# Kernel tuning notes

Measured on AMD Instinct MI355X. Metric: run time of the kernel, lower is better.

## Reference

```python
import jax, jax.numpy as jnp
import numpy as np

T, B = 384, 128
IN_DIM, HID, OUT_DIM = 512, 1024, 512


def _lstm_step(h, c, x_t, Wx, Wh, b):
    # x_t: [B, D], h/c: [B, H]; gates order: i, f, g, o
    gates = x_t @ Wx + h @ Wh + b  # [B, 4H]
    i, f, g, o = jnp.split(gates, 4, axis=-1)
    c_new = jax.nn.sigmoid(f) * c + jax.nn.sigmoid(i) * jnp.tanh(g)
    h_new = jax.nn.sigmoid(o) * jnp.tanh(c_new)
    return h_new, c_new


def setup_inputs() -> dict:
    key = jax.random.key(0)
    ks = jax.random.split(key, 9)
    s_in = 1.0 / np.sqrt(IN_DIM)
    s_h = 1.0 / np.sqrt(HID)
    s_o = 1.0 / np.sqrt(OUT_DIM)
    return {
        "x": jax.random.normal(ks[0], (T, B, IN_DIM), dtype=jnp.float32),
        "hidden_state": jnp.zeros((1, B, HID), dtype=jnp.float32),
        "cell_state": jnp.zeros((1, B, HID), dtype=jnp.float32),
        "enc_Wx": jax.random.normal(ks[1], (IN_DIM, 4 * HID), dtype=jnp.float32) * s_in,
        "enc_Wh": jax.random.normal(ks[2], (HID, 4 * HID), dtype=jnp.float32) * s_h,
        "enc_b": jnp.zeros((4 * HID,), dtype=jnp.float32),
        "dec_Wx": jax.random.normal(ks[3], (OUT_DIM, 4 * HID), dtype=jnp.float32) * s_o,
        "dec_Wh": jax.random.normal(ks[4], (HID, 4 * HID), dtype=jnp.float32) * s_h,
        "dec_b": jnp.zeros((4 * HID,), dtype=jnp.float32),
        "fc_W": jax.random.normal(ks[5], (HID, OUT_DIM), dtype=jnp.float32) * s_h,
        "fc_b": jnp.zeros((OUT_DIM,), dtype=jnp.float32),
    }


def reference(x, hidden_state, cell_state, enc_Wx, enc_Wh, enc_b,
              dec_Wx, dec_Wh, dec_b, fc_W, fc_b):
    # ---- encoder: run LSTM over T steps, keep only final hidden state ----
    h0, c0 = hidden_state[0], cell_state[0]  # [B, H]

    def enc_step(carry, x_t):
        h, c = carry
        h, c = _lstm_step(h, c, x_t, enc_Wx, enc_Wh, enc_b)
        return (h, c), None

    (h_enc, _), _ = jax.lax.scan(enc_step, (h0, c0), x)

    y0 = jnp.zeros((B, OUT_DIM), dtype=x.dtype)
    c_dec0 = jnp.zeros((B, HID), dtype=x.dtype)

    def dec_step(carry, _):
        y, h, c = carry
        h, c = _lstm_step(h, c, y, dec_Wx, dec_Wh, dec_b)
        y = jax.nn.softmax(h @ fc_W + fc_b, axis=-1)  # softmax over dim=2
        return (y, h, c), y

    _, output = jax.lax.scan(dec_step, (y0, h_enc, c_dec0), None, length=T)
    return output  # [T, B, OUT_DIM]
```

## Files before the change

kernel.cpp:

```cpp
#include <hip/hip_runtime.h>


#define TS 384

typedef __attribute__((ext_vector_type(8))) short bf16x8;
typedef __attribute__((ext_vector_type(4))) float f32x4;

#define WS_XR 4096u
#define XR_SLOT 262144u
#define WS_HP (WS_XR + 4u*XR_SLOT)
#define HP_BUF 524288u
#define WS_FPN (WS_HP + 2u*HP_BUF)
#define WS_TOTAL (WS_FPN + 2097152u)

#define MFMA __builtin_amdgcn_mfma_f32_16x16x32_bf16

__device__ __forceinline__ unsigned short bf16r(float v) {
  unsigned u = __float_as_uint(v);
  u += 0x7FFFu + ((u >> 16) & 1u);
  return (unsigned short)(u >> 16);
}
__device__ __forceinline__ float bf2f(unsigned short h) {
  return __uint_as_float(((unsigned)h) << 16);
}
__device__ __forceinline__ void split2(float v, short& hi, short& lo) {
  unsigned short h = bf16r(v);
  float r = v - bf2f(h);
  hi = (short)h; lo = (short)bf16r(r);
}
__device__ __forceinline__ float sigm(float v)  { return 1.0f / (1.0f + __expf(-v)); }
__device__ __forceinline__ float tanhfa(float v){ return 1.0f - 2.0f / (__expf(2.0f*v) + 1.0f); }

__device__ __forceinline__ void st_u64(void* p, unsigned long long v) {
  __hip_atomic_store((unsigned long long*)p, v, __ATOMIC_RELAXED, __HIP_MEMORY_SCOPE_AGENT);
}
__device__ __forceinline__ unsigned long long ld_u64(const void* p) {
  return __hip_atomic_load((const unsigned long long*)p, __ATOMIC_RELAXED, __HIP_MEMORY_SCOPE_AGENT);
}
__device__ __forceinline__ void st_u32(unsigned* p, unsigned v) {
  __hip_atomic_store(p, v, __ATOMIC_RELAXED, __HIP_MEMORY_SCOPE_AGENT);
}
__device__ __forceinline__ unsigned ld_u32(const unsigned* p) {
  return __hip_atomic_load(p, __ATOMIC_RELAXED, __HIP_MEMORY_SCOPE_AGENT);
}
__device__ __forceinline__ void st_f32(float* p, float v) {
  __hip_atomic_store(p, v, __ATOMIC_RELAXED, __HIP_MEMORY_SCOPE_AGENT);
}
__device__ __forceinline__ float ld_f32(const float* p) {
  return __hip_atomic_load(p, __ATOMIC_RELAXED, __HIP_MEMORY_SCOPE_AGENT);
}

__device__ __forceinline__ void setflag(unsigned* flag, unsigned val) {
  asm volatile("s_waitcnt vmcnt(0)" ::: "memory");
  __syncthreads();
  if (threadIdx.x == 0)
    __hip_atomic_store(flag, val, __ATOMIC_RELAXED, __HIP_MEMORY_SCOPE_AGENT);
}
__device__ __forceinline__ void hwait(const unsigned* flags, unsigned* invdone_line,
                                      bool leader, unsigned target, int* sDead) {
  if (leader) {
    if (threadIdx.x < 64) {
      const unsigned long long* q = (const unsigned long long*)(flags + threadIdx.x * 4);
      unsigned spins = 0;
      for (;;) {
        unsigned long long q0 = ld_u64(q), q1 = ld_u64(q + 1);
        bool ok = ((unsigned)q0 >= target) && ((unsigned)(q0 >> 32) >= target)
               && ((unsigned)q1 >= target) && ((unsigned)(q1 >> 32) >= target);
        if (__all(ok)) break;
        if (++spins > (1u << 20)) { if (threadIdx.x == 0) *sDead = 1; break; }
      }
    }
    if (threadIdx.x == 0) {
      __builtin_amdgcn_fence(__ATOMIC_ACQUIRE, "agent");
      st_u32(invdone_line, target);
      asm volatile("s_waitcnt vmcnt(0)" ::: "memory");
    }
  } else {
    if (threadIdx.x == 0) {
      unsigned spins = 0;
      while (ld_u32(invdone_line) < target) {
        if (++spins > (1u << 20)) { *sDead = 1; break; }
      }
      asm volatile("buffer_inv sc0" ::: "memory");
      asm volatile("s_waitcnt vmcnt(0)" ::: "memory");
    }
  }
  __syncthreads();
}
__device__ __forceinline__ void wait128(const unsigned* flags, unsigned target, int* sDead) {
  if (threadIdx.x < 64) {
    const int i = threadIdx.x;
    const bool act = (i * 4) < 128;
    const unsigned long long* q = (const unsigned long long*)(flags + i * 4);
    unsigned spins = 0;
    for (;;) {
      bool ok = true;
      if (act) {
        unsigned long long q0 = ld_u64(q), q1 = ld_u64(q + 1);
        ok = ((unsigned)q0 >= target) && ((unsigned)(q0 >> 32) >= target)
          && ((unsigned)q1 >= target) && ((unsigned)(q1 >> 32) >= target);
      }
      if (__all(ok)) break;
      if (++spins > (1u << 20)) { if (i == 0) *sDead = 1; break; }
    }
  }
  __syncthreads();
}

__device__ void load_gate_weights(const float* __restrict__ Wx, const float* __restrict__ Wh,
                                  int p, short* sBh, short* sBl) {
  for (int idx = threadIdx.x; idx < 24576; idx += 1024) {
    int j = idx & 7, l = (idx >> 3) & 63, kb = idx >> 9;
    int k = kb * 32 + ((l >> 4) << 3) + j;
    int c = l & 15;
    int gcol = (c >> 2) * 1024 + p * 4 + (c & 3);
    float wv = (k < 512) ? Wx[(size_t)k * 4096 + gcol]
                         : Wh[(size_t)(k - 512) * 4096 + gcol];
    short hi, lo; split2(wv, hi, lo);
    sBh[idx] = hi; sBl[idx] = lo;
  }
}
__device__ void load_fc_weights(const float* __restrict__ fcW, int kg, int cg,
                                short* sFh, short* sFl) {
  for (int idx = threadIdx.x; idx < 4096; idx += 1024) {
    int j = idx & 7, l = (idx >> 3) & 63, kb = idx >> 9;
    int unit = kg * 256 + kb * 32 + ((l >> 4) << 3) + j;
    int col = cg * 16 + (l & 15);
    short hi, lo; split2(fcW[(size_t)unit * 512 + col], hi, lo);
    sFh[idx] = hi; sFl[idx] = lo;
  }
}

template<int NKB, int D>
__device__ __forceinline__ void gg_pipe(const short* AH_, const short* AL_,
    const short* BH_, const short* BL_, int mt, int l,
    int kbA0, int kbB0, f32x4* acc)
{
  const bf16x8* AH = (const bf16x8*)AH_;
  const bf16x8* AL = (const bf16x8*)AL_;
  const bf16x8* BH = (const bf16x8*)BH_;
  const bf16x8* BL = (const bf16x8*)BL_;
  bf16x8 pah[D], pal[D];
  #pragma unroll
  for (int i = 0; i < D; ++i) {
    pah[i] = AH[((kbA0 + i) * 8 + mt) * 64 + l];
    pal[i] = AL[((kbA0 + i) * 8 + mt) * 64 + l];
  }
  #pragma unroll
  for (int i = 0; i < NKB; ++i) {
    bf16x8 ah = pah[i % D], al = pal[i % D];
    if (i + D < NKB) {
      pah[i % D] = AH[((kbA0 + i + D) * 8 + mt) * 64 + l];
      pal[i % D] = AL[((kbA0 + i + D) * 8 + mt) * 64 + l];
    }
    bf16x8 bh = BH[(kbB0 + i) * 64 + l];
    bf16x8 bl = BL[(kbB0 + i) * 64 + l];
    const int a = (i & 1) * 3;
    acc[a + 0] = MFMA(ah, bh, acc[a + 0], 0, 0, 0);
    acc[a + 1] = MFMA(ah, bl, acc[a + 1], 0, 0, 0);
    acc[a + 2] = MFMA(al, bh, acc[a + 2], 0, 0, 0);
  }
}
__device__ __forceinline__ void gg_finish(f32x4* acc, int kh, int mt, int l,
                                          float* LDSgate) {
  f32x4 s = (acc[0] + acc[3]) + ((acc[1] + acc[4]) + (acc[2] + acc[5]));
  const int col = l & 15, r0 = mt * 16 + ((l >> 4) << 2);
  float* plane = LDSgate + kh * 2176;
  #pragma unroll
  for (int j = 0; j < 4; ++j) plane[(r0 + j) * 17 + col] = s[j];
}

__device__ __forceinline__ void conv_x(const float* __restrict__ xsrc,
                                       short* dstH, short* dstL, int p, int tl) {
  if (tl < 32) {
    int g = p * 32 + tl;
    int l = g & 63, mt = (g >> 6) & 7, kb = g >> 9;
    int row = mt * 16 + (l & 15), k = kb * 32 + ((l >> 4) << 3);
    const float* xs = xsrc + (size_t)row * 512 + k;
    unsigned long long h64[2] = {0, 0}, l64[2] = {0, 0};
    #pragma unroll
    for (int j = 0; j < 8; ++j) {
      short hi, lo; split2(xs[j], hi, lo);
      h64[j >> 2] |= (unsigned long long)(unsigned short)hi << ((j & 3) * 16);
      l64[j >> 2] |= (unsigned long long)(unsigned short)lo << ((j & 3) * 16);
    }
    int off = g * 8;
    st_u64(dstH + off, h64[0]); st_u64(dstH + off + 4, h64[1]);
    st_u64(dstL + off, l64[0]); st_u64(dstL + off + 4, l64[1]);
  }
}

__global__ void __launch_bounds__(1024, 1)
lstm12(const float* __restrict__ x, const float* __restrict__ h0p,
       const float* __restrict__ c0p, const float* __restrict__ eWx,
       const float* __restrict__ eWh, const float* __restrict__ eb,
       const float* __restrict__ dWx, const float* __restrict__ dWh,
       const float* __restrict__ db, const float* __restrict__ fcW,
       const float* __restrict__ fcb, float* __restrict__ out,
       char* __restrict__ ws)
{
  __shared__ __align__(16) short sBh[24576], sBl[24576];
  __shared__ __align__(16) short sFh[4096], sFl[4096];
  __shared__ float LDSgate[2 * 2176];
  __shared__ unsigned hsplit[512];
  __shared__ float ybuf[512];
  __shared__ float red[16];
  __shared__ int sDead, sLeader, sXcd;

  const int p = blockIdx.x, t = threadIdx.x;
  const int w = t >> 6, l = t & 63;
  const int mt = w & 7, kh = w >> 3;
  if (t == 0) sDead = 0;

  unsigned* hflag = (unsigned*)ws;
  unsigned* yflag = (unsigned*)(ws + 1024);
  unsigned* fflag = (unsigned*)(ws + 2048);
  unsigned* elect = (unsigned*)(ws + 3264);

  if (t == 0) {
    unsigned xcd;
    asm volatile("s_getreg_b32 %0, hwreg(HW_REG_XCC_ID)" : "=s"(xcd));
    xcd &= 7u;
    sXcd = (int)xcd;
    unsigned old = __hip_atomic_fetch_add(&elect[xcd], 1u, __ATOMIC_ACQ_REL,
                                          __HIP_MEMORY_SCOPE_AGENT);
    sLeader = (old == 0u) ? 1 : 0;
  }
  __syncthreads();
  const bool leader = (sLeader != 0);
  unsigned* invd = (unsigned*)(ws + 3328 + sXcd * 64);

  short* xrH[4]; short* xrL[4];
  #pragma unroll
  for (int s4 = 0; s4 < 4; ++s4) {
    xrH[s4] = (short*)(ws + WS_XR + s4 * XR_SLOT);
    xrL[s4] = (short*)(ws + WS_XR + s4 * XR_SLOT + 131072u);
  }
  short* hpH[2]; short* hpL[2];
  #pragma unroll
  for (int b2 = 0; b2 < 2; ++b2) {
    hpH[b2] = (short*)(ws + WS_HP + b2 * HP_BUF);
    hpL[b2] = (short*)(ws + WS_HP + b2 * HP_BUF + 262144u);
  }
  float* fp = (float*)(ws + WS_FPN);

  const int row_pw = t & 127, u_pw = (t >> 7) & 3;

  load_gate_weights(eWx, eWh, p, sBh, sBl);
  conv_x(x, xrH[0], xrL[0], p, t);
  conv_x(x + 65536, xrH[1], xrL[1], p, t);
  if (t < 64) {
    int hg = p * 64 + t;
    int ll = hg & 63, mtt = (hg >> 6) & 7, hk = hg >> 9;
    int row = mtt * 16 + (ll & 15), k = hk * 32 + ((ll >> 4) << 3);
    const float* hs = h0p + (size_t)row * 1024 + k;
    unsigned long long h64[2] = {0, 0}, l64[2] = {0, 0};
    #pragma unroll
    for (int j = 0; j < 8; ++j) {
      short hi, lo; split2(hs[j], hi, lo);
      h64[j >> 2] |= (unsigned long long)(unsigned short)hi << ((j & 3) * 16);
      l64[j >> 2] |= (unsigned long long)(unsigned short)lo << ((j & 3) * 16);
    }
    int off = hg * 8;
    st_u64(hpH[0] + off, h64[0]); st_u64(hpH[0] + off + 4, h64[1]);
    st_u64(hpL[0] + off, l64[0]); st_u64(hpL[0] + off + 4, l64[1]);
  }
  float creg = 0.f, bq0 = 0.f, bq1 = 0.f, bq2 = 0.f, bq3 = 0.f;
  if (t < 512) {
    creg = c0p[(size_t)row_pw * 1024 + p * 4 + u_pw];
    bq0 = eb[0 * 1024 + p * 4 + u_pw];
    bq1 = eb[1 * 1024 + p * 4 + u_pw];
    bq2 = eb[2 * 1024 + p * 4 + u_pw];
    bq3 = eb[3 * 1024 + p * 4 + u_pw];
  }
  setflag(&hflag[p], 1u);
  hwait(hflag, invd, leader, 1u, &sDead);
  if (sDead) return;

  for (int st = 0; st < TS; ++st) {
    int rb = st & 1, wb = rb ^ 1, xs = st & 3;
    f32x4 z = {0.f, 0.f, 0.f, 0.f};
    f32x4 acc[6] = {z, z, z, z, z, z};
    gg_pipe<8, 4>(xrH[xs], xrL[xs], sBh, sBl, mt, l, kh * 8, kh * 8, acc);
    hwait(hflag, invd, leader, (unsigned)(st + 1), &sDead);
    if (sDead) return;
    gg_pipe<16, 4>(hpH[rb], hpL[rb], sBh, sBl, mt, l, kh * 16, 16 + kh * 16, acc);
    gg_finish(acc, kh, mt, l, LDSgate);
    __syncthreads();
    if (t < 512) {
      float g0 = LDSgate[row_pw * 17 + 0  + u_pw] + LDSgate[2176 + row_pw * 17 + 0  + u_pw] + bq0;
      float g1 = LDSgate[row_pw * 17 + 4  + u_pw] + LDSgate[2176 + row_pw * 17 + 4  + u_pw] + bq1;
      float g2 = LDSgate[row_pw * 17 + 8  + u_pw] + LDSgate[2176 + row_pw * 17 + 8  + u_pw] + bq2;
      float g3 = LDSgate[row_pw * 17 + 12 + u_pw] + LDSgate[2176 + row_pw * 17 + 12 + u_pw] + bq3;
      creg = sigm(g1) * creg + sigm(g0) * tanhfa(g2);
      float h = sigm(g3) * tanhfa(creg);
      short hi, lo; split2(h, hi, lo);
      hsplit[u_pw * 128 + row_pw] = ((unsigned)(unsigned short)hi << 16) | (unsigned short)lo;
    } else if (st + 2 < TS) {
      conv_x(x + (size_t)(st + 2) * 65536, xrH[(st + 2) & 3], xrL[(st + 2) & 3], p, t - 512);
    }
    __syncthreads();
    if (t < 128) {
      int r = t;
      unsigned w0 = hsplit[r], w1 = hsplit[128 + r], w2 = hsplit[256 + r], w3 = hsplit[384 + r];
      unsigned long long hi64 = (unsigned long long)(w0 >> 16)
        | ((unsigned long long)(w1 >> 16) << 16)
        | ((unsigned long long)(w2 >> 16) << 32)
        | ((unsigned long long)(w3 >> 16) << 48);
      unsigned long long lo64 = (unsigned long long)(w0 & 0xFFFFu)
        | ((unsigned long long)(w1 & 0xFFFFu) << 16)
        | ((unsigned long long)(w2 & 0xFFFFu) << 32)
        | ((unsigned long long)(w3 & 0xFFFFu) << 48);
      int hk = p >> 3, mtt = r >> 4;
      int lane_ = (((p >> 1) & 3) << 4) | (r & 15);
      int off = ((hk * 8 + mtt) * 64 + lane_) * 8 + (p & 1) * 4;
      st_u64(hpH[wb] + off, hi64);
      st_u64(hpL[wb] + off, lo64);
    }
    setflag(&hflag[p], (unsigned)(st + 2));
  }

  load_gate_weights(dWx, dWh, p, sBh, sBl);
  if (p >= 128) load_fc_weights(fcW, (p - 128) >> 5, (p - 128) & 31, sFh, sFl);
  if (t < 32) {
    int off = (p * 32 + t) * 8;
    st_u64(xrH[0] + off, 0ull); st_u64(xrH[0] + off + 4, 0ull);
    st_u64(xrL[0] + off, 0ull); st_u64(xrL[0] + off + 4, 0ull);
  }
  creg = 0.0f;
  if (t < 512) {
    bq0 = db[0 * 1024 + p * 4 + u_pw];
    bq1 = db[1 * 1024 + p * 4 + u_pw];
    bq2 = db[2 * 1024 + p * 4 + u_pw];
    bq3 = db[3 * 1024 + p * 4 + u_pw];
  }
  float fcb_r = (t < 512) ? fcb[t] : 0.f;
  setflag(&hflag[p], (unsigned)(TS + 2));

  const unsigned DB = (unsigned)(TS + 2);
  for (int st = 0; st < TS; ++st) {
    const int rb = st & 1, wb = rb ^ 1;
    f32x4 z = {0.f, 0.f, 0.f, 0.f};
    f32x4 acc[6] = {z, z, z, z, z, z};
    hwait(hflag, invd, leader, DB + (unsigned)st, &sDead);
    if (sDead) return;
    if (p >= 128) {
      const int f = p - 128, kg = f >> 5, cg = f & 31;
      if (st >= 1) {
        const bf16x8* AH = (const bf16x8*)hpH[rb];
        const bf16x8* AL = (const bf16x8*)hpL[rb];
        const bf16x8* FB = (const bf16x8*)sFh;
        const bf16x8* FL = (const bf16x8*)sFl;
        f32x4 a0 = z, a1 = z, a2 = z;
        #pragma unroll
        for (int kb = 0; kb < 4; ++kb) {
          int gkb = kg * 8 + kh * 4 + kb;
          bf16x8 ah = AH[(gkb * 8 + mt) * 64 + l];
          bf16x8 al = AL[(gkb * 8 + mt) * 64 + l];
          bf16x8 bh = FB[(kh * 4 + kb) * 64 + l];
          bf16x8 bl = FL[(kh * 4 + kb) * 64 + l];
          a0 = MFMA(ah, bh, a0, 0, 0, 0);
          a1 = MFMA(ah, bl, a1, 0, 0, 0);
          a2 = MFMA(al, bh, a2, 0, 0, 0);
        }
        f32x4 s = a0 + (a1 + a2);
        int slice = kg * 2 + kh;
        int col = cg * 16 + (l & 15), r0 = mt * 16 + ((l >> 4) << 2);
        #pragma unroll
        for (int j = 0; j < 4; ++j)
          st_f32(&fp[(size_t)(slice * 128 + r0 + j) * 512 + col], s[j]);
        setflag(&fflag[f], (unsigned)st);
      }
      gg_pipe<16, 4>(hpH[rb], hpL[rb], sBh, sBl, mt, l, kh * 16, 16 + kh * 16, acc);
      if (st >= 1) { wait128(yflag, (unsigned)st, &sDead); if (sDead) return; }
      gg_pipe<8, 4>(xrH[rb], xrL[rb], sBh, sBl, mt, l, kh * 8, kh * 8, acc);
    } else {
      gg_pipe<16, 4>(hpH[rb], hpL[rb], sBh, sBl, mt, l, kh * 16, 16 + kh * 16, acc);
      if (st >= 1) {
        wait128(fflag, (unsigned)st, &sDead);
        if (sDead) return;
        float v = 0.f, e = 0.f, mx;
        if (t < 512) {
          float tv[8];
          #pragma unroll
          for (int s8 = 0; s8 < 8; ++s8)
            tv[s8] = ld_f32(&fp[(size_t)(s8 * 128 + p) * 512 + t]);
          v = fcb_r + ((tv[0] + tv[1]) + (tv[2] + tv[3]))
                    + ((tv[4] + tv[5]) + (tv[6] + tv[7]));
          mx = v;
          #pragma unroll
          for (int o = 32; o > 0; o >>= 1) mx = fmaxf(mx, __shfl_xor(mx, o));
          if (l == 0) red[w] = mx;
        }
        __syncthreads();
        if (t < 512) {
          mx = red[0];
          #pragma unroll
          for (int i = 1; i < 8; ++i) mx = fmaxf(mx, red[i]);
          e = __expf(v - mx);
          float ss = e;
          #pragma unroll
          for (int o = 32; o > 0; o >>= 1) ss += __shfl_xor(ss, o);
          if (l == 0) red[8 + w] = ss;
        }
        __syncthreads();
        if (t < 512) {
          float ss = (red[8] + red[9]) + (red[10] + red[11])
                   + (red[12] + red[13]) + (red[14] + red[15]);
          float y = e / ss;
          st_f32(&out[((size_t)(st - 1) * 128 + p) * 512 + t], y);
          ybuf[t] = y;
        }
        __syncthreads();
        if (t < 64) {
          int kb = t >> 2, seg = t & 3;
          int k = kb * 32 + seg * 8;
          int lane_ = (seg << 4) | (p & 15), mtt = p >> 4;
          int off = ((kb * 8 + mtt) * 64 + lane_) * 8;
          unsigned long long h64[2] = {0, 0}, l64[2] = {0, 0};
          #pragma unroll
          for (int j = 0; j < 8; ++j) {
            short hi, lo; split2(ybuf[k + j], hi, lo);
            h64[j >> 2] |= (unsigned long long)(unsigned short)hi << ((j & 3) * 16);
            l64[j >> 2] |= (unsigned long long)(unsigned short)lo << ((j & 3) * 16);
          }
          st_u64(xrH[rb] + off, h64[0]); st_u64(xrH[rb] + off + 4, h64[1]);
          st_u64(xrL[rb] + off, l64[0]); st_u64(xrL[rb] + off + 4, l64[1]);
        }
        setflag(&yflag[p], (unsigned)st);
        wait128(yflag, (unsigned)st, &sDead);
        if (sDead) return;
      }
      gg_pipe<8, 4>(xrH[rb], xrL[rb], sBh, sBl, mt, l, kh * 8, kh * 8, acc);
    }
    gg_finish(acc, kh, mt, l, LDSgate);
    __syncthreads();
    if (t < 512) {
      float g0 = LDSgate[row_pw * 17 + 0  + u_pw] + LDSgate[2176 + row_pw * 17 + 0  + u_pw] + bq0;
      float g1 = LDSgate[row_pw * 17 + 4  + u_pw] + LDSgate[2176 + row_pw * 17 + 4  + u_pw] + bq1;
      float g2 = LDSgate[row_pw * 17 + 8  + u_pw] + LDSgate[2176 + row_pw * 17 + 8  + u_pw] + bq2;
      float g3 = LDSgate[row_pw * 17 + 12 + u_pw] + LDSgate[2176 + row_pw * 17 + 12 + u_pw] + bq3;
      creg = sigm(g1) * creg + sigm(g0) * tanhfa(g2);
      float h = sigm(g3) * tanhfa(creg);
      short hi, lo; split2(h, hi, lo);
      hsplit[u_pw * 128 + row_pw] = ((unsigned)(unsigned short)hi << 16) | (unsigned short)lo;
    }
    __syncthreads();
    if (t < 128) {
      int r = t;
      unsigned w0 = hsplit[r], w1 = hsplit[128 + r], w2 = hsplit[256 + r], w3 = hsplit[384 + r];
      unsigned long long hi64 = (unsigned long long)(w0 >> 16)
        | ((unsigned long long)(w1 >> 16) << 16)
        | ((unsigned long long)(w2 >> 16) << 32)
        | ((unsigned long long)(w3 >> 16) << 48);
      unsigned long long lo64 = (unsigned long long)(w0 & 0xFFFFu)
        | ((unsigned long long)(w1 & 0xFFFFu) << 16)
        | ((unsigned long long)(w2 & 0xFFFFu) << 32)
        | ((unsigned long long)(w3 & 0xFFFFu) << 48);
      int hk = p >> 3, mtt = r >> 4;
      int lane_ = (((p >> 1) & 3) << 4) | (r & 15);
      int off = ((hk * 8 + mtt) * 64 + lane_) * 8 + (p & 1) * 4;
      st_u64(hpH[wb] + off, hi64);
      st_u64(hpL[wb] + off, lo64);
    }
    setflag(&hflag[p], DB + (unsigned)(st + 1));
  }

  {
    const int rb = TS & 1;
    hwait(hflag, invd, leader, DB + (unsigned)TS, &sDead);
    if (sDead) return;
    if (p >= 128) {
      const int f = p - 128, kg = f >> 5, cg = f & 31;
      const bf16x8* AH = (const bf16x8*)hpH[rb];
      const bf16x8* AL = (const bf16x8*)hpL[rb];
      const bf16x8* FB = (const bf16x8*)sFh;
      const bf16x8* FL = (const bf16x8*)sFl;
      f32x4 z = {0.f, 0.f, 0.f, 0.f};
      f32x4 a0 = z, a1 = z, a2 = z;
      #pragma unroll
      for (int kb = 0; kb < 4; ++kb) {
        int gkb = kg * 8 + kh * 4 + kb;
        bf16x8 ah = AH[(gkb * 8 + mt) * 64 + l];
        bf16x8 al = AL[(gkb * 8 + mt) * 64 + l];
        bf16x8 bh = FB[(kh * 4 + kb) * 64 + l];
        bf16x8 bl = FL[(kh * 4 + kb) * 64 + l];
        a0 = MFMA(ah, bh, a0, 0, 0, 0);
        a1 = MFMA(ah, bl, a1, 0, 0, 0);
        a2 = MFMA(al, bh, a2, 0, 0, 0);
      }
      f32x4 s = a0 + (a1 + a2);
      int slice = kg * 2 + kh;
      int col = cg * 16 + (l & 15), r0 = mt * 16 + ((l >> 4) << 2);
      #pragma unroll
      for (int j = 0; j < 4; ++j)
        st_f32(&fp[(size_t)(slice * 128 + r0 + j) * 512 + col], s[j]);
      setflag(&fflag[f], (unsigned)TS);
    } else {
      wait128(fflag, (unsigned)TS, &sDead);
      if (sDead) return;
      float v = 0.f, e = 0.f, mx;
      if (t < 512) {
        float tv[8];
        #pragma unroll
        for (int s8 = 0; s8 < 8; ++s8)
          tv[s8] = ld_f32(&fp[(size_t)(s8 * 128 + p) * 512 + t]);
        v = fcb_r + ((tv[0] + tv[1]) + (tv[2] + tv[3]))
                  + ((tv[4] + tv[5]) + (tv[6] + tv[7]));
        mx = v;
        #pragma unroll
        for (int o = 32; o > 0; o >>= 1) mx = fmaxf(mx, __shfl_xor(mx, o));
        if (l == 0) red[w] = mx;
      }
      __syncthreads();
      if (t < 512) {
        mx = red[0];
        #pragma unroll
        for (int i = 1; i < 8; ++i) mx = fmaxf(mx, red[i]);
        e = __expf(v - mx);
        float ss = e;
        #pragma unroll
        for (int o = 32; o > 0; o >>= 1) ss += __shfl_xor(ss, o);
        if (l == 0) red[8 + w] = ss;
      }
      __syncthreads();
      if (t < 512) {
        float ss = (red[8] + red[9]) + (red[10] + red[11])
                 + (red[12] + red[13]) + (red[14] + red[15]);
        st_f32(&out[((size_t)(TS - 1) * 128 + p) * 512 + t], e / ss);
      }
    }
  }
}

extern "C" void kernel_launch(void* const* d_in, const int* in_sizes, int n_in,
                              void* d_out, int out_size, void* d_ws, size_t ws_size,
                              hipStream_t stream) {
  const float* x   = (const float*)d_in[0];
  const float* h0  = (const float*)d_in[1];
  const float* c0  = (const float*)d_in[2];
  const float* eWx = (const float*)d_in[3];
  const float* eWh = (const float*)d_in[4];
  const float* eb  = (const float*)d_in[5];
  const float* dWx = (const float*)d_in[6];
  const float* dWh = (const float*)d_in[7];
  const float* db  = (const float*)d_in[8];
  const float* fcW = (const float*)d_in[9];
  const float* fcb = (const float*)d_in[10];
  float* out = (float*)d_out;

  if (ws_size < (size_t)WS_TOTAL) {
    hipMemsetAsync(d_out, 0xFF, (size_t)out_size * sizeof(float), stream);
    return;
  }
  hipMemsetAsync(d_ws, 0, 4096, stream);
  hipLaunchKernelGGL(lstm12, dim3(256), dim3(1024), 0, stream,
                     x, h0, c0, eWx, eWh, eb, dWx, dWh, db, fcW, fcb, out,
                     (char*)d_ws);
}
```

Before: 13.74 ms.

## Split persistent LSTM across 512 blocks of 512 threads with narrower per-block slices

Repartitions the persistent cooperative LSTM kernel from 256 blocks of 1024 threads to 512 blocks of 512 threads, each owning 2 hidden units instead of 4. The K-split across two wave groups is removed so each wave covers the full K range, and the LDS weight layout is reorganised to match. FC work moves to 256 blocks, each computing two full output columns, so the softmax blocks no longer sum 8 partial slices. More blocks spread the per-step matvec across more CUs, but grid-wide flag polling now spans 512 flags, and the serial K loop per wave is longer.

```diff
diff --git a/kernel.cpp b/kernel.cpp
--- a/kernel.cpp
+++ b/kernel.cpp
@@ -6,14 +6,15 @@
 typedef __attribute__((ext_vector_type(8))) short bf16x8;
 typedef __attribute__((ext_vector_type(4))) float f32x4;
 
-#define WS_XR 4096u
+#define WS_XR 8192u
 #define XR_SLOT 262144u
 #define WS_HP (WS_XR + 4u*XR_SLOT)
 #define HP_BUF 524288u
 #define WS_FPN (WS_HP + 2u*HP_BUF)
-#define WS_TOTAL (WS_FPN + 2097152u)
+#define WS_TOTAL (WS_FPN + 262144u)
 
 #define MFMA __builtin_amdgcn_mfma_f32_16x16x32_bf16
+#define SPINCAP (1u << 22)
 
 __device__ __forceinline__ unsigned short bf16r(float v) {
   unsigned u = __float_as_uint(v);
@@ -56,30 +57,34 @@
   if (threadIdx.x == 0)
     __hip_atomic_store(flag, val, __ATOMIC_RELAXED, __HIP_MEMORY_SCOPE_AGENT);
 }
-__device__ __forceinline__ void hwait(const unsigned* flags, unsigned* invdone_line,
+__device__ __forceinline__ void hwait(const unsigned* flags, unsigned* invd,
                                       bool leader, unsigned target, int* sDead) {
+  const int t = threadIdx.x;
   if (leader) {
-    if (threadIdx.x < 64) {
-      const unsigned long long* q = (const unsigned long long*)(flags + threadIdx.x * 4);
+    if (t < 64) {
+      const unsigned long long* q = (const unsigned long long*)(flags + t * 8);
       unsigned spins = 0;
       for (;;) {
-        unsigned long long q0 = ld_u64(q), q1 = ld_u64(q + 1);
+        unsigned long long q0 = ld_u64(q),     q1 = ld_u64(q + 1);
+        unsigned long long q2 = ld_u64(q + 2), q3 = ld_u64(q + 3);
         bool ok = ((unsigned)q0 >= target) && ((unsigned)(q0 >> 32) >= target)
-               && ((unsigned)q1 >= target) && ((unsigned)(q1 >> 32) >= target);
+               && ((unsigned)q1 >= target) && ((unsigned)(q1 >> 32) >= target)
+               && ((unsigned)q2 >= target) && ((unsigned)(q2 >> 32) >= target)
+               && ((unsigned)q3 >= target) && ((unsigned)(q3 >> 32) >= target);
         if (__all(ok)) break;
-        if (++spins > (1u << 20)) { if (threadIdx.x == 0) *sDead = 1; break; }
-      }
-    }
-    if (threadIdx.x == 0) {
+        if (++spins > SPINCAP) { if (t == 0) *sDead = 1; break; }
+      }
+    }
+    if (t == 0) {
       __builtin_amdgcn_fence(__ATOMIC_ACQUIRE, "agent");
-      st_u32(invdone_line, target);
+      st_u32(invd, target);
       asm volatile("s_waitcnt vmcnt(0)" ::: "memory");
     }
   } else {
-    if (threadIdx.x == 0) {
+    if (t == 0) {
       unsigned spins = 0;
-      while (ld_u32(invdone_line) < target) {
-        if (++spins > (1u << 20)) { *sDead = 1; break; }
+      while (ld_u32(invd) < target) {
+        if (++spins > SPINCAP) { *sDead = 1; break; }
       }
       asm volatile("buffer_inv sc0" ::: "memory");
       asm volatile("s_waitcnt vmcnt(0)" ::: "memory");
@@ -87,59 +92,59 @@
   }
   __syncthreads();
 }
-__device__ __forceinline__ void wait128(const unsigned* flags, unsigned target, int* sDead) {
-  if (threadIdx.x < 64) {
-    const int i = threadIdx.x;
-    const bool act = (i * 4) < 128;
-    const unsigned long long* q = (const unsigned long long*)(flags + i * 4);
+template<int NF>
+__device__ __forceinline__ void waitN(const unsigned* flags, unsigned target, int* sDead) {
+  const int t = threadIdx.x;
+  if (t < 64) {
+    constexpr int PU = NF / 128;
+    const unsigned long long* q = (const unsigned long long*)(flags + t * (PU * 2));
     unsigned spins = 0;
     for (;;) {
       bool ok = true;
-      if (act) {
-        unsigned long long q0 = ld_u64(q), q1 = ld_u64(q + 1);
-        ok = ((unsigned)q0 >= target) && ((unsigned)(q0 >> 32) >= target)
-          && ((unsigned)q1 >= target) && ((unsigned)(q1 >> 32) >= target);
+      #pragma unroll
+      for (int i = 0; i < PU; ++i) {
+        unsigned long long v = ld_u64(q + i);
+        if (!(((unsigned)v >= target) && ((unsigned)(v >> 32) >= target))) ok = false;
       }
       if (__all(ok)) break;
-      if (++spins > (1u << 20)) { if (i == 0) *sDead = 1; break; }
+      if (++spins > SPINCAP) { if (t == 0) *sDead = 1; break; }
     }
   }
   __syncthreads();
 }
 
-__device__ void load_gate_weights(const float* __restrict__ Wx, const float* __restrict__ Wh,
-                                  int p, short* sBh, short* sBl) {
-  for (int idx = threadIdx.x; idx < 24576; idx += 1024) {
-    int j = idx & 7, l = (idx >> 3) & 63, kb = idx >> 9;
-    int k = kb * 32 + ((l >> 4) << 3) + j;
-    int c = l & 15;
-    int gcol = (c >> 2) * 1024 + p * 4 + (c & 3);
+__device__ void load_gw(const float* __restrict__ Wx, const float* __restrict__ Wh,
+                        int p, short* sBh, short* sBl) {
+  for (int idx = threadIdx.x; idx < 12288; idx += 512) {
+    int kb = idx >> 8, rem = idx & 255;
+    int c8 = rem >> 5, kk = rem & 31;
+    int k = kb * 32 + kk;
+    int gcol = (c8 >> 1) * 1024 + p * 2 + (c8 & 1);
     float wv = (k < 512) ? Wx[(size_t)k * 4096 + gcol]
                          : Wh[(size_t)(k - 512) * 4096 + gcol];
     short hi, lo; split2(wv, hi, lo);
     sBh[idx] = hi; sBl[idx] = lo;
   }
 }
-__device__ void load_fc_weights(const float* __restrict__ fcW, int kg, int cg,
-                                short* sFh, short* sFl) {
-  for (int idx = threadIdx.x; idx < 4096; idx += 1024) {
-    int j = idx & 7, l = (idx >> 3) & 63, kb = idx >> 9;
-    int unit = kg * 256 + kb * 32 + ((l >> 4) << 3) + j;
-    int col = cg * 16 + (l & 15);
+__device__ void load_fcw(const float* __restrict__ fcW, int f, short* sFh, short* sFl) {
+  for (int idx = threadIdx.x; idx < 2048; idx += 512) {
+    int kb = idx >> 6, rem = idx & 63;
+    int c = rem >> 5, kk = rem & 31;
+    int unit = kb * 32 + kk;
+    int col = f * 2 + c;
     short hi, lo; split2(fcW[(size_t)unit * 512 + col], hi, lo);
     sFh[idx] = hi; sFl[idx] = lo;
   }
 }
 
 template<int NKB, int D>
-__device__ __forceinline__ void gg_pipe(const short* AH_, const short* AL_,
+__device__ __forceinline__ void gg(const short* AH_, const short* AL_,
     const short* BH_, const short* BL_, int mt, int l,
     int kbA0, int kbB0, f32x4* acc)
 {
   const bf16x8* AH = (const bf16x8*)AH_;
   const bf16x8* AL = (const bf16x8*)AL_;
-  const bf16x8* BH = (const bf16x8*)BH_;
-  const bf16x8* BL = (const bf16x8*)BL_;
+  const int boff = ((l & 7) * 32) + ((l >> 4) << 3);
   bf16x8 pah[D], pal[D];
   #pragma unroll
   for (int i = 0; i < D; ++i) {
@@ -153,27 +158,28 @@
       pah[i % D] = AH[((kbA0 + i + D) * 8 + mt) * 64 + l];
       pal[i % D] = AL[((kbA0 + i + D) * 8 + mt) * 64 + l];
     }
-    bf16x8 bh = BH[(kbB0 + i) * 64 + l];
-    bf16x8 bl = BL[(kbB0 + i) * 64 + l];
+    bf16x8 bh = *(const bf16x8*)&BH_[(kbB0 + i) * 256 + boff];
+    bf16x8 bl = *(const bf16x8*)&BL_[(kbB0 + i) * 256 + boff];
     const int a = (i & 1) * 3;
     acc[a + 0] = MFMA(ah, bh, acc[a + 0], 0, 0, 0);
     acc[a + 1] = MFMA(ah, bl, acc[a + 1], 0, 0, 0);
     acc[a + 2] = MFMA(al, bh, acc[a + 2], 0, 0, 0);
   }
 }
-__device__ __forceinline__ void gg_finish(f32x4* acc, int kh, int mt, int l,
-                                          float* LDSgate) {
+__device__ __forceinline__ void gg_finish(f32x4* acc, int mt, int l, float* LDSgate) {
   f32x4 s = (acc[0] + acc[3]) + ((acc[1] + acc[4]) + (acc[2] + acc[5]));
-  const int col = l & 15, r0 = mt * 16 + ((l >> 4) << 2);
-  float* plane = LDSgate + kh * 2176;
-  #pragma unroll
-  for (int j = 0; j < 4; ++j) plane[(r0 + j) * 17 + col] = s[j];
+  const int col8 = l & 15;
+  if (col8 < 8) {
+    const int r0 = mt * 16 + ((l >> 4) << 2);
+    #pragma unroll
+    for (int j = 0; j < 4; ++j) LDSgate[(r0 + j) * 9 + col8] = s[j];
+  }
 }
 
 __device__ __forceinline__ void conv_x(const float* __restrict__ xsrc,
                                        short* dstH, short* dstL, int p, int tl) {
-  if (tl < 32) {
-    int g = p * 32 + tl;
+  if (tl >= 0 && tl < 16) {
+    int g = p * 16 + tl;
     int l = g & 63, mt = (g >> 6) & 7, kb = g >> 9;
     int row = mt * 16 + (l & 15), k = kb * 32 + ((l >> 4) << 3);
     const float* xs = xsrc + (size_t)row * 512 + k;
@@ -190,8 +196,8 @@
   }
 }
 
-__global__ void __launch_bounds__(1024, 1)
-lstm12(const float* __restrict__ x, const float* __restrict__ h0p,
+__global__ void __launch_bounds__(512, 4)
+lstm17(const float* __restrict__ x, const float* __restrict__ h0p,
        const float* __restrict__ c0p, const float* __restrict__ eWx,
        const float* __restrict__ eWh, const float* __restrict__ eb,
        const float* __restrict__ dWx, const float* __restrict__ dWh,
@@ -199,23 +205,23 @@
        const float* __restrict__ fcb, float* __restrict__ out,
        char* __restrict__ ws)
 {
-  __shared__ __align__(16) short sBh[24576], sBl[24576];
-  __shared__ __align__(16) short sFh[4096], sFl[4096];
-  __shared__ float LDSgate[2 * 2176];
-  __shared__ unsigned hsplit[512];
+  __shared__ __align__(16) short sBh[12288], sBl[12288];
+  __shared__ __align__(16) short sFh[2048], sFl[2048];
+  __shared__ float LDSgate[128 * 9];
+  __shared__ unsigned hsplit[256];
   __shared__ float ybuf[512];
   __shared__ float red[16];
   __shared__ int sDead, sLeader, sXcd;
 
   const int p = blockIdx.x, t = threadIdx.x;
   const int w = t >> 6, l = t & 63;
-  const int mt = w & 7, kh = w >> 3;
+  const int mt = w;
   if (t == 0) sDead = 0;
 
   unsigned* hflag = (unsigned*)ws;
-  unsigned* yflag = (unsigned*)(ws + 1024);
-  unsigned* fflag = (unsigned*)(ws + 2048);
-  unsigned* elect = (unsigned*)(ws + 3264);
+  unsigned* yflag = (unsigned*)(ws + 2048);
+  unsigned* fflag = (unsigned*)(ws + 2560);
+  unsigned* elect = (unsigned*)(ws + 3584);
 
   if (t == 0) {
     unsigned xcd;
@@ -228,7 +234,7 @@
   }
   __syncthreads();
   const bool leader = (sLeader != 0);
-  unsigned* invd = (unsigned*)(ws + 3328 + sXcd * 64);
+  unsigned* invd = (unsigned*)(ws + 3648 + sXcd * 64);
 
   short* xrH[4]; short* xrL[4];
   #pragma unroll
@@ -244,13 +250,13 @@
   }
   float* fp = (float*)(ws + WS_FPN);
 
-  const int row_pw = t & 127, u_pw = (t >> 7) & 3;
-
-  load_gate_weights(eWx, eWh, p, sBh, sBl);
+  const int row_pw = t & 127, u_pw = (t >> 7) & 1;
+
+  load_gw(eWx, eWh, p, sBh, sBl);
   conv_x(x, xrH[0], xrL[0], p, t);
-  conv_x(x + 65536, xrH[1], xrL[1], p, t);
-  if (t < 64) {
-    int hg = p * 64 + t;
+  conv_x(x + 65536, xrH[1], xrL[1], p, (t >= 16 && t < 32) ? (t - 16) : -1);
+  if (t < 32) {
+    int hg = p * 32 + t;
     int ll = hg & 63, mtt = (hg >> 6) & 7, hk = hg >> 9;
     int row = mtt * 16 + (ll & 15), k = hk * 32 + ((ll >> 4) << 3);
     const float* hs = h0p + (size_t)row * 1024 + k;
@@ -266,12 +272,11 @@
     st_u64(hpL[0] + off, l64[0]); st_u64(hpL[0] + off + 4, l64[1]);
   }
   float creg = 0.f, bq0 = 0.f, bq1 = 0.f, bq2 = 0.f, bq3 = 0.f;
-  if (t < 512) {
-    creg = c0p[(size_t)row_pw * 1024 + p * 4 + u_pw];
-    bq0 = eb[0 * 1024 + p * 4 + u_pw];
-    bq1 = eb[1 * 1024 + p * 4 + u_pw];
-    bq2 = eb[2 * 1024 + p * 4 + u_pw];
-    bq3 = eb[3 * 1024 + p * 4 + u_pw];
+  if (t < 256) {
+    int ug = p * 2 + u_pw;
+    creg = c0p[(size_t)row_pw * 1024 + ug];
+    bq0 = eb[0 * 1024 + ug]; bq1 = eb[1 * 1024 + ug];
+    bq2 = eb[2 * 1024 + ug]; bq3 = eb[3 * 1024 + ug];
   }
   setflag(&hflag[p], 1u);
   hwait(hflag, invd, leader, 1u, &sDead);
@@ -281,60 +286,54 @@
     int rb = st & 1, wb = rb ^ 1, xs = st & 3;
     f32x4 z = {0.f, 0.f, 0.f, 0.f};
     f32x4 acc[6] = {z, z, z, z, z, z};
-    gg_pipe<8, 4>(xrH[xs], xrL[xs], sBh, sBl, mt, l, kh * 8, kh * 8, acc);
+    gg<16, 4>(xrH[xs], xrL[xs], sBh, sBl, mt, l, 0, 0, acc);
     hwait(hflag, invd, leader, (unsigned)(st + 1), &sDead);
     if (sDead) return;
-    gg_pipe<16, 4>(hpH[rb], hpL[rb], sBh, sBl, mt, l, kh * 16, 16 + kh * 16, acc);
-    gg_finish(acc, kh, mt, l, LDSgate);
+    gg<32, 4>(hpH[rb], hpL[rb], sBh, sBl, mt, l, 0, 16, acc);
+    gg_finish(acc, mt, l, LDSgate);
     __syncthreads();
-    if (t < 512) {
-      float g0 = LDSgate[row_pw * 17 + 0  + u_pw] + LDSgate[2176 + row_pw * 17 + 0  + u_pw] + bq0;
-      float g1 = LDSgate[row_pw * 17 + 4  + u_pw] + LDSgate[2176 + row_pw * 17 + 4  + u_pw] + bq1;
-      float g2 = LDSgate[row_pw * 17 + 8  + u_pw] + LDSgate[2176 + row_pw * 17 + 8  + u_pw] + bq2;
-      float g3 = LDSgate[row_pw * 17 + 12 + u_pw] + LDSgate[2176 + row_pw * 17 + 12 + u_pw] + bq3;
+    if (t < 256) {
+      float g0 = LDSgate[row_pw * 9 + 0 + u_pw] + bq0;
+      float g1 = LDSgate[row_pw * 9 + 2 + u_pw] + bq1;
+      float g2 = LDSgate[row_pw * 9 + 4 + u_pw] + bq2;
+      float g3 = LDSgate[row_pw * 9 + 6 + u_pw] + bq3;
       creg = sigm(g1) * creg + sigm(g0) * tanhfa(g2);
       float h = sigm(g3) * tanhfa(creg);
       short hi, lo; split2(h, hi, lo);
       hsplit[u_pw * 128 + row_pw] = ((unsigned)(unsigned short)hi << 16) | (unsigned short)lo;
     } else if (st + 2 < TS) {
-      conv_x(x + (size_t)(st + 2) * 65536, xrH[(st + 2) & 3], xrL[(st + 2) & 3], p, t - 512);
+      conv_x(x + (size_t)(st + 2) * 65536, xrH[(st + 2) & 3], xrL[(st + 2) & 3], p, t - 256);
     }
     __syncthreads();
     if (t < 128) {
       int r = t;
-      unsigned w0 = hsplit[r], w1 = hsplit[128 + r], w2 = hsplit[256 + r], w3 = hsplit[384 + r];
-      unsigned long long hi64 = (unsigned long long)(w0 >> 16)
-        | ((unsigned long long)(w1 >> 16) << 16)
-        | ((unsigned long long)(w2 >> 16) << 32)
-        | ((unsigned long long)(w3 >> 16) << 48);
-      unsigned long long lo64 = (unsigned long long)(w0 & 0xFFFFu)
-        | ((unsigned long long)(w1 & 0xFFFFu) << 16)
-        | ((unsigned long long)(w2 & 0xFFFFu) << 32)
-        | ((unsigned long long)(w3 & 0xFFFFu) << 48);
-      int hk = p >> 3, mtt = r >> 4;
-      int lane_ = (((p >> 1) & 3) << 4) | (r & 15);
-      int off = ((hk * 8 + mtt) * 64 + lane_) * 8 + (p & 1) * 4;
-      st_u64(hpH[wb] + off, hi64);
-      st_u64(hpL[wb] + off, lo64);
+      unsigned h0v = hsplit[r], h1v = hsplit[128 + r];
+      unsigned hi32 = (h0v >> 16) | ((h1v >> 16) << 16);
+      unsigned lo32 = (h0v & 0xFFFFu) | ((h1v & 0xFFFFu) << 16);
+      int kb = p >> 4, mtt = r >> 4;
+      int lane_ = (((p >> 2) & 3) << 4) | (r & 15);
+      int j = (p * 2) & 7;
+      int off = ((kb * 8 + mtt) * 64 + lane_) * 8 + j;
+      st_u32((unsigned*)(hpH[wb] + off), hi32);
+      st_u32((unsigned*)(hpL[wb] + off), lo32);
     }
     setflag(&hflag[p], (unsigned)(st + 2));
   }
 
-  load_gate_weights(dWx, dWh, p, sBh, sBl);
-  if (p >= 128) load_fc_weights(fcW, (p - 128) >> 5, (p - 128) & 31, sFh, sFl);
-  if (t < 32) {
-    int off = (p * 32 + t) * 8;
+  load_gw(dWx, dWh, p, sBh, sBl);
+  if (p >= 256) load_fcw(fcW, p - 256, sFh, sFl);
+  if (t < 16) {
+    int off = (p * 16 + t) * 8;
     st_u64(xrH[0] + off, 0ull); st_u64(xrH[0] + off + 4, 0ull);
     st_u64(xrL[0] + off, 0ull); st_u64(xrL[0] + off + 4, 0ull);
   }
   creg = 0.0f;
-  if (t < 512) {
-    bq0 = db[0 * 1024 + p * 4 + u_pw];
-    bq1 = db[1 * 1024 + p * 4 + u_pw];
-    bq2 = db[2 * 1024 + p * 4 + u_pw];
-    bq3 = db[3 * 1024 + p * 4 + u_pw];
-  }
-  float fcb_r = (t < 512) ? fcb[t] : 0.f;
+  if (t < 256) {
+    int ug = p * 2 + u_pw;
+    bq0 = db[0 * 1024 + ug]; bq1 = db[1 * 1024 + ug];
+    bq2 = db[2 * 1024 + ug]; bq3 = db[3 * 1024 + ug];
+  }
+  float fcb_r = fcb[t];
   setflag(&hflag[p], (unsigned)(TS + 2));
 
   const unsigned DB = (unsigned)(TS + 2);
@@ -344,73 +343,66 @@
     f32x4 acc[6] = {z, z, z, z, z, z};
     hwait(hflag, invd, leader, DB + (unsigned)st, &sDead);
     if (sDead) return;
-    if (p >= 128) {
-      const int f = p - 128, kg = f >> 5, cg = f & 31;
+    if (p >= 256) {
       if (st >= 1) {
+        const int boff2 = ((l & 1) * 32) + ((l >> 4) << 3);
         const bf16x8* AH = (const bf16x8*)hpH[rb];
         const bf16x8* AL = (const bf16x8*)hpL[rb];
-        const bf16x8* FB = (const bf16x8*)sFh;
-        const bf16x8* FL = (const bf16x8*)sFl;
-        f32x4 a0 = z, a1 = z, a2 = z;
+        f32x4 a0 = z, a1 = z, a2 = z, a3 = z, a4 = z, a5 = z;
         #pragma unroll
-        for (int kb = 0; kb < 4; ++kb) {
-          int gkb = kg * 8 + kh * 4 + kb;
-          bf16x8 ah = AH[(gkb * 8 + mt) * 64 + l];
-          bf16x8 al = AL[(gkb * 8 + mt) * 64 + l];
-          bf16x8 bh = FB[(kh * 4 + kb) * 64 + l];
-          bf16x8 bl = FL[(kh * 4 + kb) * 64 + l];
-          a0 = MFMA(ah, bh, a0, 0, 0, 0);
-          a1 = MFMA(ah, bl, a1, 0, 0, 0);
-          a2 = MFMA(al, bh, a2, 0, 0, 0);
+        for (int kb = 0; kb < 32; ++kb) {
+          bf16x8 ah = AH[(kb * 8 + mt) * 64 + l];
+          bf16x8 al = AL[(kb * 8 + mt) * 64 + l];
+          bf16x8 bh = *(const bf16x8*)&sFh[kb * 64 + boff2];
+          bf16x8 bl = *(const bf16x8*)&sFl[kb * 64 + boff2];
+          if ((kb & 1) == 0) {
+            a0 = MFMA(ah, bh, a0, 0, 0, 0);
+            a1 = MFMA(ah, bl, a1, 0, 0, 0);
+            a2 = MFMA(al, bh, a2, 0, 0, 0);
+          } else {
+            a3 = MFMA(ah, bh, a3, 0, 0, 0);
+            a4 = MFMA(ah, bl, a4, 0, 0, 0);
+            a5 = MFMA(al, bh, a5, 0, 0, 0);
+          }
         }
-        f32x4 s = a0 + (a1 + a2);
-        int slice = kg * 2 + kh;
-        int col = cg * 16 + (l & 15), r0 = mt * 16 + ((l >> 4) << 2);
+        f32x4 s = (a0 + a3) + ((a1 + a4) + (a2 + a5));
+        if ((l & 15) < 2) {
+          int col = (p - 256) * 2 + (l & 1);
+          int r0 = mt * 16 + ((l >> 4) << 2);
+          #pragma unroll
+          for (int j = 0; j < 4; ++j)
+            st_f32(&fp[(size_t)(r0 + j) * 512 + col], s[j]);
+        }
+        setflag(&fflag[p - 256], (unsigned)st);
+      }
+      gg<32, 4>(hpH[rb], hpL[rb], sBh, sBl, mt, l, 0, 16, acc);
+      if (st >= 1) { waitN<128>(yflag, (unsigned)st, &sDead); if (sDead) return; }
+      gg<16, 4>(xrH[rb], xrL[rb], sBh, sBl, mt, l, 0, 0, acc);
+    } else {
+      gg<32, 4>(hpH[rb], hpL[rb], sBh, sBl, mt, l, 0, 16, acc);
+      if (p < 128 && st >= 1) {
+        waitN<256>(fflag, (unsigned)st, &sDead);
+        if (sDead) return;
+        float v = fcb_r + ld_f32(&fp[(size_t)p * 512 + t]);
+        float mx = v;
         #pragma unroll
-        for (int j = 0; j < 4; ++j)
-          st_f32(&fp[(size_t)(slice * 128 + r0 + j) * 512 + col], s[j]);
-        setflag(&fflag[f], (unsigned)st);
-      }
-      gg_pipe<16, 4>(hpH[rb], hpL[rb], sBh, sBl, mt, l, kh * 16, 16 + kh * 16, acc);
-      if (st >= 1) { wait128(yflag, (unsigned)st, &sDead); if (sDead) return; }
-      gg_pipe<8, 4>(xrH[rb], xrL[rb], sBh, sBl, mt, l, kh * 8, kh * 8, acc);
-    } else {
-      gg_pipe<16, 4>(hpH[rb], hpL[rb], sBh, sBl, mt, l, kh * 16, 16 + kh * 16, acc);
-      if (st >= 1) {
-        wait128(fflag, (unsigned)st, &sDead);
-        if (sDead) return;
-        float v = 0.f, e = 0.f, mx;
-        if (t < 512) {
-          float tv[8];
-          #pragma unroll
-          for (int s8 = 0; s8 < 8; ++s8)
-            tv[s8] = ld_f32(&fp[(size_t)(s8 * 128 + p) * 512 + t]);
-          v = fcb_r + ((tv[0] + tv[1]) + (tv[2] + tv[3]))
-                    + ((tv[4] + tv[5]) + (tv[6] + tv[7]));
-          mx = v;
-          #pragma unroll
-          for (int o = 32; o > 0; o >>= 1) mx = fmaxf(mx, __shfl_xor(mx, o));
-          if (l == 0) red[w] = mx;
-        }
+        for (int o = 32; o > 0; o >>= 1) mx = fmaxf(mx, __shfl_xor(mx, o));
+        if (l == 0) red[w] = mx;
         __syncthreads();
-        if (t < 512) {
-          mx = red[0];
-          #pragma unroll
-          for (int i = 1; i < 8; ++i) mx = fmaxf(mx, red[i]);
-          e = __expf(v - mx);
-          float ss = e;
-          #pragma unroll
-          for (int o = 32; o > 0; o >>= 1) ss += __shfl_xor(ss, o);
-          if (l == 0) red[8 + w] = ss;
-        }
+        mx = red[0];
+        #pragma unroll
+        for (int i = 1; i < 8; ++i) mx = fmaxf(mx, red[i]);
+        float e = __expf(v - mx);
+        float ss = e;
+        #pragma unroll
+        for (int o = 32; o > 0; o >>= 1) ss += __shfl_xor(ss, o);
+        if (l == 0) red[8 + w] = ss;
         __syncthreads();
-        if (t < 512) {
-          float ss = (red[8] + red[9]) + (red[10] + red[11])
-                   + (red[12] + red[13]) + (red[14] + red[15]);
-          float y = e / ss;
-          st_f32(&out[((size_t)(st - 1) * 128 + p) * 512 + t], y);
-          ybuf[t] = y;
-        }
+        ss = (red[8] + red[9]) + (red[10] + red[11])
+           + (red[12] + red[13]) + (red[14] + red[15]);
+        float y = e / ss;
+        st_f32(&out[((size_t)(st - 1) * 128 + p) * 512 + t], y);
+        ybuf[t] = y;
         __syncthreads();
         if (t < 64) {
           int kb = t >> 2, seg = t & 3;
@@ -428,18 +420,17 @@
           st_u64(xrL[rb] + off, l64[0]); st_u64(xrL[rb] + off + 4, l64[1]);
         }
         setflag(&yflag[p], (unsigned)st);
-        wait128(yflag, (unsigned)st, &sDead);
-        if (sDead) return;
-      }
-      gg_pipe<8, 4>(xrH[rb], xrL[rb], sBh, sBl, mt, l, kh * 8, kh * 8, acc);
-    }
-    gg_finish(acc, kh, mt, l, LDSgate);
+      }
+      if (st >= 1) { waitN<128>(yflag, (unsigned)st, &sDead); if (sDead) return; }
+      gg<16, 4>(xrH[rb], xrL[rb], sBh, sBl, mt, l, 0, 0, acc);
+    }
+    gg_finish(acc, mt, l, LDSgate);
     __syncthreads();
-    if (t < 512) {
-      float g0 = LDSgate[row_pw * 17 + 0  + u_pw] + LDSgate[2176 + row_pw * 17 + 0  + u_pw] + bq0;
-      float g1 = LDSgate[row_pw * 17 + 4  + u_pw] + LDSgate[2176 + row_pw * 17 + 4  + u_pw] + bq1;
-      float g2 = LDSgate[row_pw * 17 + 8  + u_pw] + LDSgate[2176 + row_pw * 17 + 8  + u_pw] + bq2;
-      float g3 = LDSgate[row_pw * 17 + 12 + u_pw] + LDSgate[2176 + row_pw * 17 + 12 + u_pw] + bq3;
+    if (t < 256) {
+      float g0 = LDSgate[row_pw * 9 + 0 + u_pw] + bq0;
+      float g1 = LDSgate[row_pw * 9 + 2 + u_pw] + bq1;
+      float g2 = LDSgate[row_pw * 9 + 4 + u_pw] + bq2;
+      float g3 = LDSgate[row_pw * 9 + 6 + u_pw] + bq3;
       creg = sigm(g1) * creg + sigm(g0) * tanhfa(g2);
       float h = sigm(g3) * tanhfa(creg);
       short hi, lo; split2(h, hi, lo);
@@ -448,20 +439,15 @@
     __syncthreads();
     if (t < 128) {
       int r = t;
-      unsigned w0 = hsplit[r], w1 = hsplit[128 + r], w2 = hsplit[256 + r], w3 = hsplit[384 + r];
-      unsigned long long hi64 = (unsigned long long)(w0 >> 16)
-        | ((unsigned long long)(w1 >> 16) << 16)
-        | ((unsigned long long)(w2 >> 16) << 32)
-        | ((unsigned long long)(w3 >> 16) << 48);
-      unsigned long long lo64 = (unsigned long long)(w0 & 0xFFFFu)
-        | ((unsigned long long)(w1 & 0xFFFFu) << 16)
-        | ((unsigned long long)(w2 & 0xFFFFu) << 32)
-        | ((unsigned long long)(w3 & 0xFFFFu) << 48);
-      int hk = p >> 3, mtt = r >> 4;
-      int lane_ = (((p >> 1) & 3) << 4) | (r & 15);
-      int off = ((hk * 8 + mtt) * 64 + lane_) * 8 + (p & 1) * 4;
-      st_u64(hpH[wb] + off, hi64);
-      st_u64(hpL[wb] + off, lo64);
+      unsigned h0v = hsplit[r], h1v = hsplit[128 + r];
+      unsigned hi32 = (h0v >> 16) | ((h1v >> 16) << 16);
+      unsigned lo32 = (h0v & 0xFFFFu) | ((h1v & 0xFFFFu) << 16);
+      int kb = p >> 4, mtt = r >> 4;
+      int lane_ = (((p >> 2) & 3) << 4) | (r & 15);
+      int j = (p * 2) & 7;
+      int off = ((kb * 8 + mtt) * 64 + lane_) * 8 + j;
+      st_u32((unsigned*)(hpH[wb] + off), hi32);
+      st_u32((unsigned*)(hpL[wb] + off), lo32);
     }
     setflag(&hflag[p], DB + (unsigned)(st + 1));
   }
@@ -470,65 +456,58 @@
     const int rb = TS & 1;
     hwait(hflag, invd, leader, DB + (unsigned)TS, &sDead);
     if (sDead) return;
-    if (p >= 128) {
-      const int f = p - 128, kg = f >> 5, cg = f & 31;
+    if (p >= 256) {
+      const int boff2 = ((l & 1) * 32) + ((l >> 4) << 3);
       const bf16x8* AH = (const bf16x8*)hpH[rb];
       const bf16x8* AL = (const bf16x8*)hpL[rb];
-      const bf16x8* FB = (const bf16x8*)sFh;
-      const bf16x8* FL = (const bf16x8*)sFl;
       f32x4 z = {0.f, 0.f, 0.f, 0.f};
-      f32x4 a0 = z, a1 = z, a2 = z;
+      f32x4 a0 = z, a1 = z, a2 = z, a3 = z, a4 = z, a5 = z;
       #pragma unroll
-      for (int kb = 0; kb < 4; ++kb) {
-        int gkb = kg * 8 + kh * 4 + kb;
-        bf16x8 ah = AH[(gkb * 8 + mt) * 64 + l];
-        bf16x8 al = AL[(gkb * 8 + mt) * 64 + l];
-        bf16x8 bh = FB[(kh * 4 + kb) * 64 + l];
-        bf16x8 bl = FL[(kh * 4 + kb) * 64 + l];
-        a0 = MFMA(ah, bh, a0, 0, 0, 0);
-        a1 = MFMA(ah, bl, a1, 0, 0, 0);
-        a2 = MFMA(al, bh, a2, 0, 0, 0);
-      }
-      f32x4 s = a0 + (a1 + a2);
-      int slice = kg * 2 + kh;
-      int col = cg * 16 + (l & 15), r0 = mt * 16 + ((l >> 4) << 2);
+      for (int kb = 0; kb < 32; ++kb) {
+        bf16x8 ah = AH[(kb * 8 + mt) * 64 + l];
+        bf16x8 al = AL[(kb * 8 + mt) * 64 + l];
+        bf16x8 bh = *(const bf16x8*)&sFh[kb * 64 + boff2];
+        bf16x8 bl = *(const bf16x8*)&sFl[kb * 64 + boff2];
+        if ((kb & 1) == 0) {
+          a0 = MFMA(ah, bh, a0, 0, 0, 0);
+          a1 = MFMA(ah, bl, a1, 0, 0, 0);
+          a2 = MFMA(al, bh, a2, 0, 0, 0);
+        } else {
+          a3 = MFMA(ah, bh, a3, 0, 0, 0);
+          a4 = MFMA(ah, bl, a4, 0, 0, 0);
+          a5 = MFMA(al, bh, a5, 0, 0, 0);
+        }
+      }
+      f32x4 s = (a0 + a3) + ((a1 + a4) + (a2 + a5));
+      if ((l & 15) < 2) {
+        int col = (p - 256) * 2 + (l & 1);
+        int r0 = mt * 16 + ((l >> 4) << 2);
+        #pragma unroll
+        for (int j = 0; j < 4; ++j)
+          st_f32(&fp[(size_t)(r0 + j) * 512 + col], s[j]);
+      }
+      setflag(&fflag[p - 256], (unsigned)TS);
+    } else if (p < 128) {
+      waitN<256>(fflag, (unsigned)TS, &sDead);
+      if (sDead) return;
+      float v = fcb_r + ld_f32(&fp[(size_t)p * 512 + t]);
+      float mx = v;
       #pragma unroll
-      for (int j = 0; j < 4; ++j)
-        st_f32(&fp[(size_t)(slice * 128 + r0 + j) * 512 + col], s[j]);
-      setflag(&fflag[f], (unsigned)TS);
-    } else {
-      wait128(fflag, (unsigned)TS, &sDead);
-      if (sDead) return;
-      float v = 0.f, e = 0.f, mx;
-      if (t < 512) {
-        float tv[8];
-        #pragma unroll
-        for (int s8 = 0; s8 < 8; ++s8)
-          tv[s8] = ld_f32(&fp[(size_t)(s8 * 128 + p) * 512 + t]);
-        v = fcb_r + ((tv[0] + tv[1]) + (tv[2] + tv[3]))
-                  + ((tv[4] + tv[5]) + (tv[6] + tv[7]));
-        mx = v;
-        #pragma unroll
-        for (int o = 32; o > 0; o >>= 1) mx = fmaxf(mx, __shfl_xor(mx, o));
-        if (l == 0) red[w] = mx;
-      }
+      for (int o = 32; o > 0; o >>= 1) mx = fmaxf(mx, __shfl_xor(mx, o));
+      if (l == 0) red[w] = mx;
       __syncthreads();
-      if (t < 512) {
-        mx = red[0];
-        #pragma unroll
-        for (int i = 1; i < 8; ++i) mx = fmaxf(mx, red[i]);
-        e = __expf(v - mx);
-        float ss = e;
-        #pragma unroll
-        for (int o = 32; o > 0; o >>= 1) ss += __shfl_xor(ss, o);
-        if (l == 0) red[8 + w] = ss;
-      }
+      mx = red[0];
+      #pragma unroll
+      for (int i = 1; i < 8; ++i) mx = fmaxf(mx, red[i]);
+      float e = __expf(v - mx);
+      float ss = e;
+      #pragma unroll
+      for (int o = 32; o > 0; o >>= 1) ss += __shfl_xor(ss, o);
+      if (l == 0) red[8 + w] = ss;
       __syncthreads();
-      if (t < 512) {
-        float ss = (red[8] + red[9]) + (red[10] + red[11])
-                 + (red[12] + red[13]) + (red[14] + red[15]);
-        st_f32(&out[((size_t)(TS - 1) * 128 + p) * 512 + t], e / ss);
-      }
+      ss = (red[8] + red[9]) + (red[10] + red[11])
+         + (red[12] + red[13]) + (red[14] + red[15]);
+      st_f32(&out[((size_t)(TS - 1) * 128 + p) * 512 + t], e / ss);
     }
   }
 }
@@ -550,11 +529,11 @@
   float* out = (float*)d_out;
 
   if (ws_size < (size_t)WS_TOTAL) {
-    hipMemsetAsync(d_out, 0xFF, (size_t)out_size * sizeof(float), stream);
+    (void)hipMemsetAsync(d_out, 0xFF, (size_t)out_size * sizeof(float), stream);
     return;
   }
-  hipMemsetAsync(d_ws, 0, 4096, stream);
-  hipLaunchKernelGGL(lstm12, dim3(256), dim3(1024), 0, stream,
+  (void)hipMemsetAsync(d_ws, 0, 8192, stream);
+  hipLaunchKernelGGL(lstm17, dim3(512), dim3(512), 0, stream,
                      x, h0, c0, eWx, eWh, eb, dWx, dWh, db, fcW, fcb, out,
                      (char*)d_ws);
 }
```

Result: slower. 23.21 ms (+69.0%).
